# Optimization experiments

Hardware: AMD Instinct MI355X
Metric: run time of the kernel (lower is better)

## Reference

```python
import jax, jax.numpy as jnp
import numpy as np
from jax import lax

# config constants (match init_kwargs)
SEQ_LEN = 512
PRED_LEN = 96
ENC_IN = 64
D_MODEL = 128
E_LAYERS = 2
GRAPH_SCALE = 16
GRAPH_RANK = 8
TCN_KERNEL = 3
TCN_DILATION = 2
BATCH = 16


def setup_inputs() -> dict:
    key = jax.random.key(0)
    ks = jax.random.split(key, 12)
    s = 0.02
    inp = {
        "x_enc": jax.random.normal(ks[0], (BATCH, SEQ_LEN, ENC_IN), jnp.float32),
        "x_mark_enc": jnp.zeros((BATCH, SEQ_LEN, 4), jnp.float32),
        "x_dec": jnp.zeros((BATCH, PRED_LEN, ENC_IN), jnp.float32),
        "x_mark_dec": jnp.zeros((BATCH, PRED_LEN, 4), jnp.float32),
        # value embedding (scalar -> d_model)
        "w_emb": jax.random.normal(ks[1], (1, D_MODEL), jnp.float32) * s,
        "b_emb": jnp.zeros((D_MODEL,), jnp.float32),
        # stacked dilated causal conv layers [L, K, Cin, Cout]
        "conv_w": jax.random.normal(ks[2], (E_LAYERS, TCN_KERNEL, D_MODEL, D_MODEL), jnp.float32) * s,
        "conv_b": jnp.zeros((E_LAYERS, D_MODEL), jnp.float32),
        # low-rank graph generator projections
        "gg_w1": jax.random.normal(ks[3], (D_MODEL, GRAPH_RANK), jnp.float32) * s,
        "gg_b1": jnp.zeros((GRAPH_RANK,), jnp.float32),
        "gg_w2": jax.random.normal(ks[4], (D_MODEL, GRAPH_RANK), jnp.float32) * s,
        "gg_b2": jnp.zeros((GRAPH_RANK,), jnp.float32),
        # head: Linear(d_model * num_tokens, pred_len)
        "head_w": jax.random.normal(ks[5], (D_MODEL * SEQ_LEN, PRED_LEN), jnp.float32) * s,
        "head_b": jnp.zeros((PRED_LEN,), jnp.float32),
    }
    return inp


def _tcn(x_enc, w_emb, b_emb, conv_w, conv_b):
    # x_enc: [B, L, N] -> channel-independent per-variable encoding -> [B, N, L, D]
    B, L, N = x_enc.shape
    h = x_enc.transpose(0, 2, 1).reshape(B * N, L, 1) @ w_emb + b_emb  # [B*N, L, D]
    for i in range(conv_w.shape[0]):
        dil = TCN_DILATION ** i
        pad = (TCN_KERNEL - 1) * dil
        hp = jnp.pad(h, ((0, 0), (pad, 0), (0, 0)))  # causal left pad
        y = lax.conv_general_dilated(
            hp, conv_w[i], window_strides=(1,), padding="VALID",
            rhs_dilation=(dil,), dimension_numbers=("NWC", "WIO", "NWC"),
        ) + conv_b[i]
        h = jax.nn.gelu(y) + h  # residual
    return h.reshape(B, N, L, -1)


def _forward(x_enc, w_emb, b_emb, conv_w, conv_b, gg_w1, gg_b1, gg_w2, gg_b2, head_w, head_b):
    h_time = _tcn(x_enc, w_emb, b_emb, conv_w, conv_b)  # [B, N, L, D]
    B, N, L, D = h_time.shape
    S = L // GRAPH_SCALE  # number of segments (L divisible by scale)
    h_seg = h_time.reshape(B, N, S, GRAPH_SCALE, D)
    z = h_seg.mean(axis=3)  # [B, N, S, D] segment summaries
    # low-rank graph generation for all segments at once
    e1 = z @ gg_w1 + gg_b1  # [B, N, S, r]
    e2 = z @ gg_w2 + gg_b2
    scores = jnp.einsum("bnsr,bmsr->bsnm", e1, e2) / jnp.asarray(np.sqrt(GRAPH_RANK), z.dtype)
    adj = jax.nn.softmax(scores, axis=-1)  # [B, S, N, N] row-stochastic
    # adjacency temporal-smoothness regularizer: sum_s mean|adj_s - adj_{s-1}|
    reg = jnp.sum(jnp.mean(jnp.abs(adj[:, 1:] - adj[:, :-1]), axis=(0, 2, 3)))
    # graph-weighted feature mixing per segment
    h_mix = jnp.einsum("bsnm,bmscd->bnscd", adj, h_seg).reshape(B, N, L, D)
    # head over flattened (token, dim)
    out = h_mix.reshape(B, N, L * D) @ head_w + head_b  # [B, N, pred_len]
    return out.transpose(0, 2, 1), reg  # [B, pred_len, N]


def reference(x_enc, x_mark_enc, x_dec, x_mark_dec, w_emb, b_emb, conv_w, conv_b,
              gg_w1, gg_b1, gg_w2, gg_b2, head_w, head_b):
    # x_mark_enc / x_dec / x_mark_dec are unused by forecast path (faithful to source)
    return _forward(x_enc, w_emb, b_emb, conv_w, conv_b, gg_w1, gg_b1, gg_w2, gg_b2, head_w, head_b)
```

## Files before the change

### kernel.cpp

```cpp
#include <hip/hip_runtime.h>
#include <hip/hip_bf16.h>


#define BATCH 16
#define SEQ 512
#define NVAR 64
#define DM 128
#define SEG 32
#define SCL 16
#define RNK 8
#define PRED 96
#define BN (BATCH * NVAR)
#define ROWLEN (SEQ * DM)

typedef unsigned short ushort_t;
typedef __attribute__((ext_vector_type(8))) short short8;
typedef __attribute__((ext_vector_type(4))) float f32x4;

__device__ inline float bf2f(ushort_t u) {
    union { unsigned int i; float f; } x;
    x.i = ((unsigned int)u) << 16;
    return x.f;
}
__device__ inline ushort_t f2bf(float f) {
    union { float f; unsigned int i; } u;
    u.f = f;
    unsigned int x = u.i;
    return (ushort_t)((x + 0x7fffu + ((x >> 16) & 1u)) >> 16);
}
__device__ inline unsigned int pkbf(float a, float b) {
    __hip_bfloat162 h = __float22bfloat162_rn(make_float2(a, b));
    union { __hip_bfloat162 h2; unsigned int u; } c;
    c.h2 = h;
    return c.u;
}
__device__ inline float blo(unsigned int u) {
    union { unsigned int i; float f; } x;
    x.i = u << 16;
    return x.f;
}
__device__ inline float bhi(unsigned int u) {
    union { unsigned int i; float f; } x;
    x.i = u & 0xFFFF0000u;
    return x.f;
}
__device__ inline float gelu_fast(float x) {
    float x2 = x * x;
    float t2 = x * fmaf(-0.10294854f, x2, -2.3022584f);
    float e;
    asm("v_exp_f32 %0, %1" : "=v"(e) : "v"(t2));
    return x * __builtin_amdgcn_rcpf(1.0f + e);
}

__global__ __launch_bounds__(256) void prep(
    const float* __restrict__ conv_w, const float* __restrict__ w_emb,
    const float* __restrict__ b_emb, const float* __restrict__ conv_b,
    const float* __restrict__ head_w, const float* __restrict__ head_b,
    ushort_t* __restrict__ WTf, float* __restrict__ Acoef,
    float* __restrict__ Bias3, ushort_t* __restrict__ HWf,
    float* __restrict__ out, float* __restrict__ regacc) {
    __shared__ float ts[32 * 97];
    int bid = blockIdx.x;
    if (bid == 0 && threadIdx.x == 0) regacc[0] = 0.f;
    if (bid < 512) {
        int bx = bid >> 7, ci = bid & 127;
        if (threadIdx.x < 128) {
            int co = threadIdx.x;
            if (bx < 3) {
                int kt = ci >> 5, quad = (ci >> 3) & 3, j = ci & 7;
                int ng = co >> 4, col = co & 15;
                int lane = quad * 16 + col;
                WTf[((((size_t)bx * 4 + kt) * 8 + ng) * 64 + lane) * 8 + j] =
                    f2bf(conv_w[(size_t)(3 + bx) * 16384 + (size_t)ci * 128 + co]);
            } else if (ci == 0) {
                float a0 = 0.f, a1 = 0.f, a2 = 0.f, c0 = 0.f, c1 = 0.f, c2 = 0.f;
                for (int k = 0; k < 128; ++k) {
                    float we = w_emb[k], be = b_emb[k];
                    float w0 = conv_w[((size_t)(0 * 128 + k)) * 128 + co];
                    float w1 = conv_w[((size_t)(1 * 128 + k)) * 128 + co];
                    float w2 = conv_w[((size_t)(2 * 128 + k)) * 128 + co];
                    a0 += we * w0; c0 += be * w0;
                    a1 += we * w1; c1 += be * w1;
                    a2 += we * w2; c2 += be * w2;
                }
                Acoef[0 * 128 + co] = a0;
                Acoef[1 * 128 + co] = a1;
                Acoef[2 * 128 + co] = a2;
                float b0 = conv_b[co];
                Bias3[0 * 128 + co] = b0 + c2;
                Bias3[1 * 128 + co] = b0 + c1 + c2;
                Bias3[2 * 128 + co] = b0 + c0 + c1 + c2;
            }
        }
    } else if (bid < 2560) {
        int k32p = bid - 512;
        const float* src = head_w + (size_t)k32p * 32 * 96;
        for (int idx = threadIdx.x; idx < 3072; idx += 256) {
            int kk = idx / 96, p = idx - kk * 96;
            ts[kk * 97 + p] = src[idx];
        }
        __syncthreads();
        unsigned int* ob32 =
            reinterpret_cast<unsigned int*>(HWf + (size_t)k32p * 3072);
        for (int odx = threadIdx.x; odx < 1536; odx += 256) {
            int p = odx >> 4, kk = (odx & 15) * 2;
            ob32[odx] = pkbf(ts[kk * 97 + p], ts[(kk + 1) * 97 + p]);
        }
    } else {
        int idx = (bid - 2560) * 256 + threadIdx.x;
        if (idx < BATCH * PRED * NVAR) {
            int p = (idx >> 6) % PRED;
            out[idx] = head_b[p];
        }
    }
}

__global__ __launch_bounds__(256, 4) void tcn_mfma(
    const float* __restrict__ x, const float* __restrict__ w_emb,
    const float* __restrict__ b_emb, const float* __restrict__ Acoef,
    const float* __restrict__ Bias3, const ushort_t* __restrict__ WTf,
    const float* __restrict__ conv_b,
    const float* __restrict__ gw1, const float* __restrict__ gb1,
    const float* __restrict__ gw2, const float* __restrict__ gb2,
    ushort_t* __restrict__ h2, float* __restrict__ e1, float* __restrict__ e2) {
    __shared__ __align__(16) ushort_t h1s[68 * 136];
    __shared__ float xs[70];
    __shared__ float zbuf[4 * 136];

    int bn = blockIdx.x;
    int b = bn >> 6, n = bn & 63;
    int chunk = blockIdx.y;
    int l0 = chunk * 64;
    int tid = threadIdx.x;

    {
        const float* xb = x + (size_t)b * SEQ * NVAR + n;
        if (tid < 70) {
            int l = l0 - 6 + tid;
            xs[tid] = (l >= 0) ? xb[(size_t)l * NVAR] : 0.0f;
        }
    }
    __syncthreads();

    {
        int dp = (tid & 63) * 2;
        float2 A0 = *reinterpret_cast<const float2*>(&Acoef[0 * 128 + dp]);
        float2 A1 = *reinterpret_cast<const float2*>(&Acoef[1 * 128 + dp]);
        float2 A2 = *reinterpret_cast<const float2*>(&Acoef[2 * 128 + dp]);
        float2 BF = *reinterpret_cast<const float2*>(&Bias3[2 * 128 + dp]);
        float2 we2 = *reinterpret_cast<const float2*>(&w_emb[dp]);
        float2 be2 = *reinterpret_cast<const float2*>(&b_emb[dp]);
#pragma unroll
        for (int i = 0; i < 17; ++i) {
            int row = (tid >> 6) + 4 * i;
            int l = l0 - 4 + row;
            unsigned int pk = 0;
            if (l >= 0) {
                float x0 = xs[row], x1 = xs[row + 1], x2 = xs[row + 2];
                float2 bias = BF;
                if (l < 2)
                    bias = *reinterpret_cast<const float2*>(&Bias3[l * 128 + dp]);
                float y0 = fmaf(x0, A0.x, fmaf(x1, A1.x, fmaf(x2, A2.x, bias.x)));
                float y1 = fmaf(x0, A0.y, fmaf(x1, A1.y, fmaf(x2, A2.y, bias.y)));
                float r0 = gelu_fast(y0) + fmaf(x2, we2.x, be2.x);
                float r1 = gelu_fast(y1) + fmaf(x2, we2.y, be2.y);
                pk = pkbf(r0, r1);
            }
            *reinterpret_cast<unsigned int*>(&h1s[row * 136 + dp]) = pk;
        }
    }
    __syncthreads();

    int lane = tid & 63;
    int wv = tid >> 6;
    int quad = lane >> 4;
    int col = lane & 15;
    int cobase = wv * 32;

    f32x4 acc2[4][2];
#pragma unroll
    for (int mt = 0; mt < 4; ++mt)
#pragma unroll
        for (int nt = 0; nt < 2; ++nt)
            acc2[mt][nt] = (f32x4){0.f, 0.f, 0.f, 0.f};

#pragma unroll
    for (int tap = 0; tap < 3; ++tap) {
        short8 wf0[4], wf1[4];
#pragma unroll
        for (int kt = 0; kt < 4; ++kt) {
            const ushort_t* bp =
                WTf + ((((size_t)tap * 4 + kt) * 8 + wv * 2) * 64 + lane) * 8;
            wf0[kt] = *(const short8*)bp;
            wf1[kt] = *(const short8*)(bp + 512);
        }
#pragma unroll
        for (int kt = 0; kt < 4; ++kt) {
            int kc = kt * 32 + quad * 8;
#pragma unroll
            for (int mt = 0; mt < 4; ++mt) {
                short8 hf = *(const short8*)&h1s[(mt * 16 + col + 2 * tap) * 136 + kc];
                acc2[mt][0] = __builtin_amdgcn_mfma_f32_16x16x32_bf16(wf0[kt], hf, acc2[mt][0], 0, 0, 0);
                acc2[mt][1] = __builtin_amdgcn_mfma_f32_16x16x32_bf16(wf1[kt], hf, acc2[mt][1], 0, 0, 0);
            }
        }
    }

    {
        uint2 res[4][2];
#pragma unroll
        for (int mt = 0; mt < 4; ++mt) {
            int li = mt * 16 + col;
#pragma unroll
            for (int nt = 0; nt < 2; ++nt) {
                int co = cobase + nt * 16 + quad * 4;
                res[mt][nt] = *reinterpret_cast<const uint2*>(
                    &h1s[(li + 4) * 136 + co]);
            }
        }
        __syncthreads();
        float4 bias[2];
        bias[0] = *reinterpret_cast<const float4*>(&conv_b[DM + cobase + quad * 4]);
        bias[1] = *reinterpret_cast<const float4*>(&conv_b[DM + cobase + 16 + quad * 4]);
#pragma unroll
        for (int mt = 0; mt < 4; ++mt) {
            int li = mt * 16 + col;
#pragma unroll
            for (int nt = 0; nt < 2; ++nt) {
                int co = cobase + nt * 16 + quad * 4;
                float h0 = gelu_fast(acc2[mt][nt][0] + bias[nt].x) + blo(res[mt][nt].x);
                float h1 = gelu_fast(acc2[mt][nt][1] + bias[nt].y) + bhi(res[mt][nt].x);
                float h2v = gelu_fast(acc2[mt][nt][2] + bias[nt].z) + blo(res[mt][nt].y);
                float h3 = gelu_fast(acc2[mt][nt][3] + bias[nt].w) + bhi(res[mt][nt].y);
                uint2 pk;
                pk.x = pkbf(h0, h1);
                pk.y = pkbf(h2v, h3);
                *reinterpret_cast<uint2*>(&h1s[li * 136 + co]) = pk;
            }
        }
    }
    __syncthreads();

    {
        ushort_t* orow = h2 + (size_t)bn * ROWLEN + (size_t)l0 * 128;
#pragma unroll
        for (int i = 0; i < 4; ++i) {
            int q = tid + 256 * i;
            int row = q >> 4, c8 = (q & 15) * 8;
            *(short8*)&orow[row * 128 + c8] = *(const short8*)&h1s[row * 136 + c8];
        }
    }
    {
        int sl = tid >> 6;
        int dp = (tid & 63) * 2;
        float a0 = 0.0f, a1 = 0.0f;
#pragma unroll
        for (int c = 0; c < SCL; ++c) {
            unsigned int u = *reinterpret_cast<const unsigned int*>(
                &h1s[(sl * 16 + c) * 136 + dp]);
            a0 += blo(u);
            a1 += bhi(u);
        }
        zbuf[sl * 136 + dp] = a0 * 0.0625f;
        zbuf[sl * 136 + dp + 1] = a1 * 0.0625f;
    }
    __syncthreads();
    {
        int outi = tid >> 2;
        int part = tid & 3;
        int sl = outi >> 4;
        int which = (outi >> 3) & 1;
        int r = outi & 7;
        const float* w = which ? gw2 : gw1;
        float a = 0.0f;
#pragma unroll 8
        for (int i = 0; i < 32; ++i) {
            int d = i * 4 + part;
            a += zbuf[sl * 136 + d] * w[d * RNK + r];
        }
        a += __shfl_xor(a, 1, 64);
        a += __shfl_xor(a, 2, 64);
        if (part == 0) {
            a += (which ? gb2 : gb1)[r];
            int s = chunk * 4 + sl;
            (which ? e2 : e1)[(((size_t)b * SEG + s) * NVAR + n) * RNK + r] = a;
        }
    }
}

__global__ __launch_bounds__(256) void g_out(
    const ushort_t* __restrict__ h2, const ushort_t* __restrict__ HWf,
    const float* __restrict__ e1, const float* __restrict__ e2,
    float* __restrict__ out, float* __restrict__ regacc) {
    __shared__ __align__(16) ushort_t As[2][64 * 72];
    __shared__ __align__(16) float Gs[96][66];
    __shared__ float e1s[2][64][9];
    __shared__ float e2s[2][64][9];
    __shared__ float wsum[4];
    float* adjn = reinterpret_cast<float*>(As);

    int b = blockIdx.x, s = blockIdx.y;
    int tid = threadIdx.x;
    int lane = tid & 63, wv = tid >> 6;
    int quad = lane >> 4, col = lane & 15;
    int mh = wv & 1;
    int ph = wv >> 1;
    int p0 = ph * 48 + col;

    for (int idx = tid; idx < 1024; idx += 256) {
        int j = idx >> 9, mm = (idx >> 3) & 63, r = idx & 7;
        int ss = s - 1 + j;
        float v1 = 0.f, v2 = 0.f;
        if (ss >= 0) {
            size_t o = (((size_t)b * SEG + ss) * NVAR + mm) * RNK + r;
            v1 = e1[o];
            v2 = e2[o];
        }
        e1s[j][mm][r] = v1;
        e2s[j][mm][r] = v2;
    }

    int arow = tid >> 2, akq = (tid & 3) * 16;
    const ushort_t* aptr =
        h2 + (size_t)(b * 64 + arow) * ROWLEN + (size_t)s * 2048 + akq;
    const ushort_t* hb =
        HWf + (size_t)s * 196608 + (size_t)p0 * 32 + quad * 8;

    f32x4 acc[3][2];
#pragma unroll
    for (int i = 0; i < 3; ++i)
#pragma unroll
        for (int j = 0; j < 2; ++j) acc[i][j] = (f32x4){0.f, 0.f, 0.f, 0.f};

    short8 pa0 = *(const short8*)aptr;
    short8 pa1 = *(const short8*)(aptr + 8);
    short8 pf[2][2][3];
#pragma unroll
    for (int kk = 0; kk < 2; ++kk)
#pragma unroll
        for (int i = 0; i < 3; ++i)
            pf[0][kk][i] = *(const short8*)(hb + kk * 3072 + i * 512);
    *(short8*)&As[0][arow * 72 + akq] = pa0;
    *(short8*)&As[0][arow * 72 + akq + 8] = pa1;
    __syncthreads();

#pragma unroll
    for (int kt = 0; kt < 32; ++kt) {
        const int par = kt & 1;
        if (kt < 31) {
            const ushort_t* ap = aptr + (kt + 1) * 64;
            pa0 = *(const short8*)ap;
            pa1 = *(const short8*)(ap + 8);
            const ushort_t* fb = hb + (size_t)(kt + 1) * 6144;
#pragma unroll
            for (int kk = 0; kk < 2; ++kk)
#pragma unroll
                for (int i = 0; i < 3; ++i)
                    pf[par ^ 1][kk][i] =
                        *(const short8*)(fb + kk * 3072 + i * 512);
        }
#pragma unroll
        for (int kk = 0; kk < 2; ++kk) {
            int kc = kk * 32 + quad * 8;
#pragma unroll
            for (int j = 0; j < 2; ++j) {
                short8 bnfr =
                    *(const short8*)&As[par][(mh * 32 + j * 16 + col) * 72 + kc];
#pragma unroll
                for (int i = 0; i < 3; ++i)
                    acc[i][j] = __builtin_amdgcn_mfma_f32_16x16x32_bf16(
                        pf[par][kk][i], bnfr, acc[i][j], 0, 0, 0);
            }
        }
        if (kt < 31) {
            *(short8*)&As[par ^ 1][arow * 72 + akq] = pa0;
            *(short8*)&As[par ^ 1][arow * 72 + akq + 8] = pa1;
        }
        __syncthreads();
    }

#pragma unroll
    for (int i = 0; i < 3; ++i)
#pragma unroll
        for (int j = 0; j < 2; ++j)
#pragma unroll
            for (int r = 0; r < 4; ++r)
                Gs[ph * 48 + i * 16 + quad * 4 + r][mh * 32 + j * 16 + col] =
                    acc[i][j][r];

    float regsum = 0.0f;
    for (int t = 0; t < 16; ++t) {
        int nl = wv * 16 + t;
        float scC = 0.0f, scP = 0.0f;
#pragma unroll
        for (int r = 0; r < 8; ++r) {
            scC += e1s[1][nl][r] * e2s[1][lane][r];
            scP += e1s[0][nl][r] * e2s[0][lane][r];
        }
        scC *= 0.35355339059327373f;
        scP *= 0.35355339059327373f;
        float mxC = scC, mxP = scP;
        for (int off = 32; off; off >>= 1) {
            mxC = fmaxf(mxC, __shfl_xor(mxC, off, 64));
            mxP = fmaxf(mxP, __shfl_xor(mxP, off, 64));
        }
        float exC = __expf(scC - mxC), exP = __expf(scP - mxP);
        float smC = exC, smP = exP;
        for (int off = 32; off; off >>= 1) {
            smC += __shfl_xor(smC, off, 64);
            smP += __shfl_xor(smP, off, 64);
        }
        float aC = exC * __builtin_amdgcn_rcpf(smC);
        if (s > 0) regsum += fabsf(aC - exP * __builtin_amdgcn_rcpf(smP));
        adjn[nl * 66 + lane] = aC;
    }
    __syncthreads();

    {
        int pg = tid >> 4;
        int ng = tid & 15;
        float ao[6][4];
#pragma unroll
        for (int j = 0; j < 6; ++j)
#pragma unroll
            for (int i = 0; i < 4; ++i) ao[j][i] = 0.f;
#pragma unroll 4
        for (int m = 0; m < 64; m += 2) {
            float2 av[4];
#pragma unroll
            for (int i = 0; i < 4; ++i)
                av[i] = *reinterpret_cast<const float2*>(
                    &adjn[(ng * 4 + i) * 66 + m]);
#pragma unroll
            for (int j = 0; j < 6; ++j) {
                float2 g = *reinterpret_cast<const float2*>(&Gs[pg * 6 + j][m]);
#pragma unroll
                for (int i = 0; i < 4; ++i)
                    ao[j][i] = fmaf(g.x, av[i].x, fmaf(g.y, av[i].y, ao[j][i]));
            }
        }
#pragma unroll
        for (int j = 0; j < 6; ++j)
#pragma unroll
            for (int i = 0; i < 4; ++i)
                atomicAdd(&out[((size_t)b * PRED + pg * 6 + j) * NVAR +
                               ng * 4 + i],
                          ao[j][i]);
    }
    for (int off = 32; off; off >>= 1) regsum += __shfl_xor(regsum, off, 64);
    if (lane == 0) wsum[wv] = regsum;
    __syncthreads();
    if (tid == 0)
        atomicAdd(regacc, wsum[0] + wsum[1] + wsum[2] + wsum[3]);
}

__global__ void fin(const float* __restrict__ regacc, float* __restrict__ out,
                    int out_size) {
    out[out_size - 1] = regacc[0] * (1.0f / 65536.0f);
}

extern "C" void kernel_launch(void* const* d_in, const int* in_sizes, int n_in,
                              void* d_out, int out_size, void* d_ws,
                              size_t ws_size, hipStream_t stream) {
    const float* x_enc  = (const float*)d_in[0];
    const float* w_emb  = (const float*)d_in[4];
    const float* b_emb  = (const float*)d_in[5];
    const float* conv_w = (const float*)d_in[6];
    const float* conv_b = (const float*)d_in[7];
    const float* gg_w1  = (const float*)d_in[8];
    const float* gg_b1  = (const float*)d_in[9];
    const float* gg_w2  = (const float*)d_in[10];
    const float* gg_b2  = (const float*)d_in[11];
    const float* head_w = (const float*)d_in[12];
    const float* head_b = (const float*)d_in[13];
    float* out = (float*)d_out;

    char* ws = (char*)d_ws;
    ushort_t* h2   = (ushort_t*)(ws);
    float* e1      = (float*)(ws + 134217728);
    float* e2      = (float*)(ws + 135266304);
    ushort_t* WTf  = (ushort_t*)(ws + 136314880);
    float* Acoef   = (float*)(ws + 136413184);
    float* Bias3   = (float*)(ws + 136414720);
    ushort_t* HWf  = (ushort_t*)(ws + 136416256);
    float* regacc  = (float*)(ws + 157286400);

    prep<<<2944, 256, 0, stream>>>(
        conv_w, w_emb, b_emb, conv_b, head_w, head_b,
        WTf, Acoef, Bias3, HWf, out, regacc);
    tcn_mfma<<<dim3(BN, SEQ / 64), 256, 0, stream>>>(
        x_enc, w_emb, b_emb, Acoef, Bias3, WTf, conv_b,
        gg_w1, gg_b1, gg_w2, gg_b2, h2, e1, e2);
    g_out<<<dim3(BATCH, SEG), 256, 0, stream>>>(
        h2, HWf, e1, e2, out, regacc);
    fin<<<1, 1, 0, stream>>>(regacc, out, out_size);
}
```

Baseline: 307.9 us.

## Move head-weight conversion into TCN launch and double K tile in g_out

The head_w transpose and bf16 conversion, along with the output bias init, move out of the prep kernel into extra grid rows (y=8,9) of the TCN kernel. This leaves prep as a small conv-weight kernel and lets the head-weight work overlap with TCN compute. In g_out the K step per iteration doubles from 64 to 128, halving barrier count at the cost of more registers and shared memory. The grid is also flattened to 1D with segment-fastest ordering. The extra blocks in the TCN grid share its LDS allocation and launch bounds.

```diff
diff --git a/kernel.cpp b/kernel.cpp
--- a/kernel.cpp
+++ b/kernel.cpp
@@ -52,66 +52,39 @@
     return x * __builtin_amdgcn_rcpf(1.0f + e);
 }
 
-__global__ __launch_bounds__(256) void prep(
+__global__ __launch_bounds__(128) void prep_wt(
     const float* __restrict__ conv_w, const float* __restrict__ w_emb,
     const float* __restrict__ b_emb, const float* __restrict__ conv_b,
-    const float* __restrict__ head_w, const float* __restrict__ head_b,
     ushort_t* __restrict__ WTf, float* __restrict__ Acoef,
-    float* __restrict__ Bias3, ushort_t* __restrict__ HWf,
-    float* __restrict__ out, float* __restrict__ regacc) {
-    __shared__ float ts[32 * 97];
+    float* __restrict__ Bias3, float* __restrict__ regacc) {
     int bid = blockIdx.x;
     if (bid == 0 && threadIdx.x == 0) regacc[0] = 0.f;
-    if (bid < 512) {
-        int bx = bid >> 7, ci = bid & 127;
-        if (threadIdx.x < 128) {
-            int co = threadIdx.x;
-            if (bx < 3) {
-                int kt = ci >> 5, quad = (ci >> 3) & 3, j = ci & 7;
-                int ng = co >> 4, col = co & 15;
-                int lane = quad * 16 + col;
-                WTf[((((size_t)bx * 4 + kt) * 8 + ng) * 64 + lane) * 8 + j] =
-                    f2bf(conv_w[(size_t)(3 + bx) * 16384 + (size_t)ci * 128 + co]);
-            } else if (ci == 0) {
-                float a0 = 0.f, a1 = 0.f, a2 = 0.f, c0 = 0.f, c1 = 0.f, c2 = 0.f;
-                for (int k = 0; k < 128; ++k) {
-                    float we = w_emb[k], be = b_emb[k];
-                    float w0 = conv_w[((size_t)(0 * 128 + k)) * 128 + co];
-                    float w1 = conv_w[((size_t)(1 * 128 + k)) * 128 + co];
-                    float w2 = conv_w[((size_t)(2 * 128 + k)) * 128 + co];
-                    a0 += we * w0; c0 += be * w0;
-                    a1 += we * w1; c1 += be * w1;
-                    a2 += we * w2; c2 += be * w2;
-                }
-                Acoef[0 * 128 + co] = a0;
-                Acoef[1 * 128 + co] = a1;
-                Acoef[2 * 128 + co] = a2;
-                float b0 = conv_b[co];
-                Bias3[0 * 128 + co] = b0 + c2;
-                Bias3[1 * 128 + co] = b0 + c1 + c2;
-                Bias3[2 * 128 + co] = b0 + c0 + c1 + c2;
-            }
-        }
-    } else if (bid < 2560) {
-        int k32p = bid - 512;
-        const float* src = head_w + (size_t)k32p * 32 * 96;
-        for (int idx = threadIdx.x; idx < 3072; idx += 256) {
-            int kk = idx / 96, p = idx - kk * 96;
-            ts[kk * 97 + p] = src[idx];
-        }
-        __syncthreads();
-        unsigned int* ob32 =
-            reinterpret_cast<unsigned int*>(HWf + (size_t)k32p * 3072);
-        for (int odx = threadIdx.x; odx < 1536; odx += 256) {
-            int p = odx >> 4, kk = (odx & 15) * 2;
-            ob32[odx] = pkbf(ts[kk * 97 + p], ts[(kk + 1) * 97 + p]);
-        }
-    } else {
-        int idx = (bid - 2560) * 256 + threadIdx.x;
-        if (idx < BATCH * PRED * NVAR) {
-            int p = (idx >> 6) % PRED;
-            out[idx] = head_b[p];
-        }
+    int bx = bid >> 7, ci = bid & 127;
+    int co = threadIdx.x;
+    if (bx < 3) {
+        int kt = ci >> 5, quad = (ci >> 3) & 3, j = ci & 7;
+        int ng = co >> 4, col = co & 15;
+        int lane = quad * 16 + col;
+        WTf[((((size_t)bx * 4 + kt) * 8 + ng) * 64 + lane) * 8 + j] =
+            f2bf(conv_w[(size_t)(3 + bx) * 16384 + (size_t)ci * 128 + co]);
+    } else if (ci == 0) {
+        float a0 = 0.f, a1 = 0.f, a2 = 0.f, c0 = 0.f, c1 = 0.f, c2 = 0.f;
+        for (int k = 0; k < 128; ++k) {
+            float we = w_emb[k], be = b_emb[k];
+            float w0 = conv_w[((size_t)(0 * 128 + k)) * 128 + co];
+            float w1 = conv_w[((size_t)(1 * 128 + k)) * 128 + co];
+            float w2 = conv_w[((size_t)(2 * 128 + k)) * 128 + co];
+            a0 += we * w0; c0 += be * w0;
+            a1 += we * w1; c1 += be * w1;
+            a2 += we * w2; c2 += be * w2;
+        }
+        Acoef[0 * 128 + co] = a0;
+        Acoef[1 * 128 + co] = a1;
+        Acoef[2 * 128 + co] = a2;
+        float b0 = conv_b[co];
+        Bias3[0 * 128 + co] = b0 + c2;
+        Bias3[1 * 128 + co] = b0 + c1 + c2;
+        Bias3[2 * 128 + co] = b0 + c0 + c1 + c2;
     }
 }
 
@@ -122,16 +95,49 @@
     const float* __restrict__ conv_b,
     const float* __restrict__ gw1, const float* __restrict__ gb1,
     const float* __restrict__ gw2, const float* __restrict__ gb2,
-    ushort_t* __restrict__ h2, float* __restrict__ e1, float* __restrict__ e2) {
+    const float* __restrict__ head_w, const float* __restrict__ head_b,
+    ushort_t* __restrict__ h2, float* __restrict__ e1, float* __restrict__ e2,
+    ushort_t* __restrict__ HWf, float* __restrict__ out) {
     __shared__ __align__(16) ushort_t h1s[68 * 136];
     __shared__ float xs[70];
     __shared__ float zbuf[4 * 136];
+
+    int tid = threadIdx.x;
+
+    if (blockIdx.y == 8) {
+        float* ts = reinterpret_cast<float*>(h1s);
+#pragma unroll
+        for (int u = 0; u < 2; ++u) {
+            int k32p = blockIdx.x * 2 + u;
+            const float* src = head_w + (size_t)k32p * 3072;
+            for (int idx = tid; idx < 3072; idx += 256) {
+                int kk = idx / 96, p = idx - kk * 96;
+                ts[kk * 97 + p] = src[idx];
+            }
+            __syncthreads();
+            unsigned int* ob32 =
+                reinterpret_cast<unsigned int*>(HWf + (size_t)k32p * 3072);
+            for (int odx = tid; odx < 1536; odx += 256) {
+                int p = odx >> 4, kk = (odx & 15) * 2;
+                ob32[odx] = pkbf(ts[kk * 97 + p], ts[(kk + 1) * 97 + p]);
+            }
+            __syncthreads();
+        }
+        return;
+    }
+    if (blockIdx.y == 9) {
+        int idx = blockIdx.x * 256 + tid;
+        if (blockIdx.x < 384 && idx < BATCH * PRED * NVAR) {
+            int p = (idx >> 6) % PRED;
+            out[idx] = head_b[p];
+        }
+        return;
+    }
 
     int bn = blockIdx.x;
     int b = bn >> 6, n = bn & 63;
     int chunk = blockIdx.y;
     int l0 = chunk * 64;
-    int tid = threadIdx.x;
 
     {
         const float* xb = x + (size_t)b * SEQ * NVAR + n;
@@ -292,14 +298,15 @@
     const ushort_t* __restrict__ h2, const ushort_t* __restrict__ HWf,
     const float* __restrict__ e1, const float* __restrict__ e2,
     float* __restrict__ out, float* __restrict__ regacc) {
-    __shared__ __align__(16) ushort_t As[2][64 * 72];
+    __shared__ __align__(16) ushort_t As[2][64 * 136];
     __shared__ __align__(16) float Gs[96][66];
     __shared__ float e1s[2][64][9];
     __shared__ float e2s[2][64][9];
     __shared__ float wsum[4];
     float* adjn = reinterpret_cast<float*>(As);
 
-    int b = blockIdx.x, s = blockIdx.y;
+    int bid = blockIdx.x;
+    int s = bid & 31, b = bid >> 5;
     int tid = threadIdx.x;
     int lane = tid & 63, wv = tid >> 6;
     int quad = lane >> 4, col = lane & 15;
@@ -320,7 +327,8 @@
         e2s[j][mm][r] = v2;
     }
 
-    int arow = tid >> 2, akq = (tid & 3) * 16;
+    int arow = tid >> 2;
+    int akq = (tid & 3) * 32;
     const ushort_t* aptr =
         h2 + (size_t)(b * 64 + arow) * ROWLEN + (size_t)s * 2048 + akq;
     const ushort_t* hb =
@@ -332,49 +340,59 @@
 #pragma unroll
         for (int j = 0; j < 2; ++j) acc[i][j] = (f32x4){0.f, 0.f, 0.f, 0.f};
 
-    short8 pa0 = *(const short8*)aptr;
-    short8 pa1 = *(const short8*)(aptr + 8);
-    short8 pf[2][2][3];
-#pragma unroll
-    for (int kk = 0; kk < 2; ++kk)
-#pragma unroll
-        for (int i = 0; i < 3; ++i)
-            pf[0][kk][i] = *(const short8*)(hb + kk * 3072 + i * 512);
-    *(short8*)&As[0][arow * 72 + akq] = pa0;
-    *(short8*)&As[0][arow * 72 + akq + 8] = pa1;
-    __syncthreads();
-
-#pragma unroll
-    for (int kt = 0; kt < 32; ++kt) {
-        const int par = kt & 1;
-        if (kt < 31) {
-            const ushort_t* ap = aptr + (kt + 1) * 64;
-            pa0 = *(const short8*)ap;
-            pa1 = *(const short8*)(ap + 8);
-            const ushort_t* fb = hb + (size_t)(kt + 1) * 6144;
-#pragma unroll
-            for (int kk = 0; kk < 2; ++kk)
-#pragma unroll
-                for (int i = 0; i < 3; ++i)
-                    pf[par ^ 1][kk][i] =
-                        *(const short8*)(fb + kk * 3072 + i * 512);
-        }
-#pragma unroll
-        for (int kk = 0; kk < 2; ++kk) {
-            int kc = kk * 32 + quad * 8;
-#pragma unroll
-            for (int j = 0; j < 2; ++j) {
-                short8 bnfr =
-                    *(const short8*)&As[par][(mh * 32 + j * 16 + col) * 72 + kc];
-#pragma unroll
-                for (int i = 0; i < 3; ++i)
-                    acc[i][j] = __builtin_amdgcn_mfma_f32_16x16x32_bf16(
-                        pf[par][kk][i], bnfr, acc[i][j], 0, 0, 0);
-            }
-        }
-        if (kt < 31) {
-            *(short8*)&As[par ^ 1][arow * 72 + akq] = pa0;
-            *(short8*)&As[par ^ 1][arow * 72 + akq + 8] = pa1;
+    short8 pa[4];
+    short8 pf[2][2][2][3];
+#pragma unroll
+    for (int j = 0; j < 4; ++j) pa[j] = *(const short8*)(aptr + j * 8);
+#pragma unroll
+    for (int tk = 0; tk < 2; ++tk)
+#pragma unroll
+        for (int kk = 0; kk < 2; ++kk)
+#pragma unroll
+            for (int i = 0; i < 3; ++i)
+                pf[0][tk][kk][i] =
+                    *(const short8*)(hb + tk * 6144 + kk * 3072 + i * 512);
+#pragma unroll
+    for (int j = 0; j < 4; ++j)
+        *(short8*)&As[0][arow * 136 + akq + j * 8] = pa[j];
+    __syncthreads();
+
+#pragma unroll
+    for (int t = 0; t < 16; ++t) {
+        const int par = t & 1;
+        if (t < 15) {
+            const ushort_t* ap = aptr + (t + 1) * 128;
+#pragma unroll
+            for (int j = 0; j < 4; ++j) pa[j] = *(const short8*)(ap + j * 8);
+            const ushort_t* fb = hb + (size_t)(t + 1) * 12288;
+#pragma unroll
+            for (int tk = 0; tk < 2; ++tk)
+#pragma unroll
+                for (int kk = 0; kk < 2; ++kk)
+#pragma unroll
+                    for (int i = 0; i < 3; ++i)
+                        pf[par ^ 1][tk][kk][i] = *(const short8*)(
+                            fb + tk * 6144 + kk * 3072 + i * 512);
+        }
+#pragma unroll
+        for (int tk = 0; tk < 2; ++tk)
+#pragma unroll
+            for (int kk = 0; kk < 2; ++kk) {
+                int kc = tk * 64 + kk * 32 + quad * 8;
+#pragma unroll
+                for (int j = 0; j < 2; ++j) {
+                    short8 bnfr = *(const short8*)&As[par][
+                        (mh * 32 + j * 16 + col) * 136 + kc];
+#pragma unroll
+                    for (int i = 0; i < 3; ++i)
+                        acc[i][j] = __builtin_amdgcn_mfma_f32_16x16x32_bf16(
+                            pf[par][tk][kk][i], bnfr, acc[i][j], 0, 0, 0);
+                }
+            }
+        if (t < 15) {
+#pragma unroll
+            for (int j = 0; j < 4; ++j)
+                *(short8*)&As[par ^ 1][arow * 136 + akq + j * 8] = pa[j];
         }
         __syncthreads();
     }
@@ -485,13 +503,11 @@
     ushort_t* HWf  = (ushort_t*)(ws + 136416256);
     float* regacc  = (float*)(ws + 157286400);
 
-    prep<<<2944, 256, 0, stream>>>(
-        conv_w, w_emb, b_emb, conv_b, head_w, head_b,
-        WTf, Acoef, Bias3, HWf, out, regacc);
-    tcn_mfma<<<dim3(BN, SEQ / 64), 256, 0, stream>>>(
+    prep_wt<<<512, 128, 0, stream>>>(
+        conv_w, w_emb, b_emb, conv_b, WTf, Acoef, Bias3, regacc);
+    tcn_mfma<<<dim3(BN, 10), 256, 0, stream>>>(
         x_enc, w_emb, b_emb, Acoef, Bias3, WTf, conv_b,
-        gg_w1, gg_b1, gg_w2, gg_b2, h2, e1, e2);
-    g_out<<<dim3(BATCH, SEG), 256, 0, stream>>>(
-        h2, HWf, e1, e2, out, regacc);
+        gg_w1, gg_b1, gg_w2, gg_b2, head_w, head_b, h2, e1, e2, HWf, out);
+    g_out<<<512, 256, 0, stream>>>(h2, HWf, e1, e2, out, regacc);
     fin<<<1, 1, 0, stream>>>(regacc, out, out_size);
 }
```

New measurement: 303.9 us. Within noise of the previous version (-1.3%).

## Load g_out A operand directly from global into registers, drop LDS staging

Applied to the files above, without the earlier changes.

The g_out GEMM no longer stages the h2 tile through double-buffered shared memory. Each wave loads its MFMA B-fragments straight from global memory into registers, with a two-deep register prefetch over 16 larger k-steps. This removes the per-iteration LDS writes and barriers, and the launch grid is flattened to 1D with the segment index varying fastest. In exchange, each h2 element is now read by more than one wave, which raises global/L2 traffic and register pressure.

```diff
diff --git a/kernel.cpp b/kernel.cpp
--- a/kernel.cpp
+++ b/kernel.cpp
@@ -292,14 +292,14 @@
     const ushort_t* __restrict__ h2, const ushort_t* __restrict__ HWf,
     const float* __restrict__ e1, const float* __restrict__ e2,
     float* __restrict__ out, float* __restrict__ regacc) {
-    __shared__ __align__(16) ushort_t As[2][64 * 72];
     __shared__ __align__(16) float Gs[96][66];
+    __shared__ __align__(16) float adjn[64][66];
     __shared__ float e1s[2][64][9];
     __shared__ float e2s[2][64][9];
     __shared__ float wsum[4];
-    float* adjn = reinterpret_cast<float*>(As);
-
-    int b = blockIdx.x, s = blockIdx.y;
+
+    int bid = blockIdx.x;
+    int s = bid & 31, b = bid >> 5;
     int tid = threadIdx.x;
     int lane = tid & 63, wv = tid >> 6;
     int quad = lane >> 4, col = lane & 15;
@@ -320,9 +320,9 @@
         e2s[j][mm][r] = v2;
     }
 
-    int arow = tid >> 2, akq = (tid & 3) * 16;
-    const ushort_t* aptr =
-        h2 + (size_t)(b * 64 + arow) * ROWLEN + (size_t)s * 2048 + akq;
+    const ushort_t* a0 = h2 +
+        (size_t)(b * 64 + mh * 32 + col) * ROWLEN + (size_t)s * 2048 + quad * 8;
+    const ushort_t* a1 = a0 + (size_t)16 * ROWLEN;
     const ushort_t* hb =
         HWf + (size_t)s * 196608 + (size_t)p0 * 32 + quad * 8;
 
@@ -332,51 +332,53 @@
 #pragma unroll
         for (int j = 0; j < 2; ++j) acc[i][j] = (f32x4){0.f, 0.f, 0.f, 0.f};
 
-    short8 pa0 = *(const short8*)aptr;
-    short8 pa1 = *(const short8*)(aptr + 8);
-    short8 pf[2][2][3];
-#pragma unroll
-    for (int kk = 0; kk < 2; ++kk)
-#pragma unroll
-        for (int i = 0; i < 3; ++i)
-            pf[0][kk][i] = *(const short8*)(hb + kk * 3072 + i * 512);
-    *(short8*)&As[0][arow * 72 + akq] = pa0;
-    *(short8*)&As[0][arow * 72 + akq + 8] = pa1;
-    __syncthreads();
-
-#pragma unroll
-    for (int kt = 0; kt < 32; ++kt) {
-        const int par = kt & 1;
-        if (kt < 31) {
-            const ushort_t* ap = aptr + (kt + 1) * 64;
-            pa0 = *(const short8*)ap;
-            pa1 = *(const short8*)(ap + 8);
-            const ushort_t* fb = hb + (size_t)(kt + 1) * 6144;
-#pragma unroll
-            for (int kk = 0; kk < 2; ++kk)
-#pragma unroll
-                for (int i = 0; i < 3; ++i)
-                    pf[par ^ 1][kk][i] =
-                        *(const short8*)(fb + kk * 3072 + i * 512);
-        }
+    short8 pa[2][2][4];
+    short8 pf[2][2][2][3];
+#pragma unroll
+    for (int tk = 0; tk < 2; ++tk)
 #pragma unroll
         for (int kk = 0; kk < 2; ++kk) {
-            int kc = kk * 32 + quad * 8;
-#pragma unroll
-            for (int j = 0; j < 2; ++j) {
-                short8 bnfr =
-                    *(const short8*)&As[par][(mh * 32 + j * 16 + col) * 72 + kc];
-#pragma unroll
-                for (int i = 0; i < 3; ++i)
-                    acc[i][j] = __builtin_amdgcn_mfma_f32_16x16x32_bf16(
-                        pf[par][kk][i], bnfr, acc[i][j], 0, 0, 0);
-            }
-        }
-        if (kt < 31) {
-            *(short8*)&As[par ^ 1][arow * 72 + akq] = pa0;
-            *(short8*)&As[par ^ 1][arow * 72 + akq + 8] = pa1;
-        }
-        __syncthreads();
+            int ko = tk * 64 + kk * 32;
+            pa[0][0][tk * 2 + kk] = *(const short8*)(a0 + ko);
+            pa[0][1][tk * 2 + kk] = *(const short8*)(a1 + ko);
+#pragma unroll
+            for (int i = 0; i < 3; ++i)
+                pf[0][tk][kk][i] =
+                    *(const short8*)(hb + tk * 6144 + kk * 3072 + i * 512);
+        }
+
+#pragma unroll
+    for (int t = 0; t < 16; ++t) {
+        const int par = t & 1;
+        if (t < 15) {
+            const ushort_t* an0 = a0 + (t + 1) * 128;
+            const ushort_t* an1 = a1 + (t + 1) * 128;
+            const ushort_t* fb = hb + (size_t)(t + 1) * 12288;
+#pragma unroll
+            for (int tk = 0; tk < 2; ++tk)
+#pragma unroll
+                for (int kk = 0; kk < 2; ++kk) {
+                    int ko = tk * 64 + kk * 32;
+                    pa[par ^ 1][0][tk * 2 + kk] = *(const short8*)(an0 + ko);
+                    pa[par ^ 1][1][tk * 2 + kk] = *(const short8*)(an1 + ko);
+#pragma unroll
+                    for (int i = 0; i < 3; ++i)
+                        pf[par ^ 1][tk][kk][i] = *(const short8*)(
+                            fb + tk * 6144 + kk * 3072 + i * 512);
+                }
+        }
+#pragma unroll
+        for (int tk = 0; tk < 2; ++tk)
+#pragma unroll
+            for (int kk = 0; kk < 2; ++kk) {
+                const int f = tk * 2 + kk;
+#pragma unroll
+                for (int j = 0; j < 2; ++j)
+#pragma unroll
+                    for (int i = 0; i < 3; ++i)
+                        acc[i][j] = __builtin_amdgcn_mfma_f32_16x16x32_bf16(
+                            pf[par][tk][kk][i], pa[par][j][f], acc[i][j], 0, 0, 0);
+            }
     }
 
 #pragma unroll
@@ -387,6 +389,7 @@
             for (int r = 0; r < 4; ++r)
                 Gs[ph * 48 + i * 16 + quad * 4 + r][mh * 32 + j * 16 + col] =
                     acc[i][j][r];
+    __syncthreads();
 
     float regsum = 0.0f;
     for (int t = 0; t < 16; ++t) {
@@ -412,7 +415,7 @@
         }
         float aC = exC * __builtin_amdgcn_rcpf(smC);
         if (s > 0) regsum += fabsf(aC - exP * __builtin_amdgcn_rcpf(smP));
-        adjn[nl * 66 + lane] = aC;
+        adjn[nl][lane] = aC;
     }
     __syncthreads();
 
@@ -430,7 +433,7 @@
 #pragma unroll
             for (int i = 0; i < 4; ++i)
                 av[i] = *reinterpret_cast<const float2*>(
-                    &adjn[(ng * 4 + i) * 66 + m]);
+                    &adjn[ng * 4 + i][m]);
 #pragma unroll
             for (int j = 0; j < 6; ++j) {
                 float2 g = *reinterpret_cast<const float2*>(&Gs[pg * 6 + j][m]);
@@ -491,7 +494,6 @@
     tcn_mfma<<<dim3(BN, SEQ / 64), 256, 0, stream>>>(
         x_enc, w_emb, b_emb, Acoef, Bias3, WTf, conv_b,
         gg_w1, gg_b1, gg_w2, gg_b2, h2, e1, e2);
-    g_out<<<dim3(BATCH, SEG), 256, 0, stream>>>(
-        h2, HWf, e1, e2, out, regacc);
+    g_out<<<512, 256, 0, stream>>>(h2, HWf, e1, e2, out, regacc);
     fin<<<1, 1, 0, stream>>>(regacc, out, out_size);
 }
```

New measurement: 327.6 us. 6.4% more time.

## Split g_out reduction over two K halves to double grid size

Applied to the files above, without the earlier changes.

The g_out kernel now launches 1024 blocks instead of 512, with each block handling half of a segment's K range (kh). It uses 128-wide K tiles with a 136-element stride, and the Gs, As and adjn buffers share one shared-memory region. The e2 values are held in registers rather than shared memory, and the previous-segment softmax used for the regularizer is computed only by the kh==0 block. The goal is more parallelism and better CU occupancy on the head GEMM. In exchange, the adjacency softmax is computed twice and out receives twice as many atomic adds.

```diff
diff --git a/kernel.cpp b/kernel.cpp
--- a/kernel.cpp
+++ b/kernel.cpp
@@ -292,14 +292,16 @@
     const ushort_t* __restrict__ h2, const ushort_t* __restrict__ HWf,
     const float* __restrict__ e1, const float* __restrict__ e2,
     float* __restrict__ out, float* __restrict__ regacc) {
-    __shared__ __align__(16) ushort_t As[2][64 * 72];
-    __shared__ __align__(16) float Gs[96][66];
+    __shared__ __align__(16) char smem[42240];
     __shared__ float e1s[2][64][9];
-    __shared__ float e2s[2][64][9];
     __shared__ float wsum[4];
-    float* adjn = reinterpret_cast<float*>(As);
-
-    int b = blockIdx.x, s = blockIdx.y;
+    ushort_t* As0 = reinterpret_cast<ushort_t*>(smem);
+    ushort_t* As1 = As0 + 64 * 136;
+    float* Gs = reinterpret_cast<float*>(smem);
+    float* adjn = reinterpret_cast<float*>(smem + 25344);
+
+    int bid = blockIdx.x;
+    int s = bid & 31, b = (bid >> 5) & 15, kh = bid >> 9;
     int tid = threadIdx.x;
     int lane = tid & 63, wv = tid >> 6;
     int quad = lane >> 4, col = lane & 15;
@@ -307,24 +309,35 @@
     int ph = wv >> 1;
     int p0 = ph * 48 + col;
 
+    float e2r[2][8];
+#pragma unroll
+    for (int j = 0; j < 2; ++j) {
+        int ss = s - 1 + j;
+        if (ss >= 0) {
+            const float* p =
+                &e2[(((size_t)b * SEG + ss) * NVAR + lane) * RNK];
+            float4 v0 = *reinterpret_cast<const float4*>(p);
+            float4 v1 = *reinterpret_cast<const float4*>(p + 4);
+            e2r[j][0] = v0.x; e2r[j][1] = v0.y; e2r[j][2] = v0.z; e2r[j][3] = v0.w;
+            e2r[j][4] = v1.x; e2r[j][5] = v1.y; e2r[j][6] = v1.z; e2r[j][7] = v1.w;
+        } else {
+#pragma unroll
+            for (int r = 0; r < 8; ++r) e2r[j][r] = 0.0f;
+        }
+    }
     for (int idx = tid; idx < 1024; idx += 256) {
-        int j = idx >> 9, mm = (idx >> 3) & 63, r = idx & 7;
+        int j = idx >> 9, nl = (idx >> 3) & 63, r = idx & 7;
         int ss = s - 1 + j;
-        float v1 = 0.f, v2 = 0.f;
-        if (ss >= 0) {
-            size_t o = (((size_t)b * SEG + ss) * NVAR + mm) * RNK + r;
-            v1 = e1[o];
-            v2 = e2[o];
-        }
-        e1s[j][mm][r] = v1;
-        e2s[j][mm][r] = v2;
-    }
-
-    int arow = tid >> 2, akq = (tid & 3) * 16;
-    const ushort_t* aptr =
-        h2 + (size_t)(b * 64 + arow) * ROWLEN + (size_t)s * 2048 + akq;
-    const ushort_t* hb =
-        HWf + (size_t)s * 196608 + (size_t)p0 * 32 + quad * 8;
+        e1s[j][nl][r] = (ss >= 0)
+            ? e1[(((size_t)b * SEG + ss) * NVAR + nl) * RNK + r] : 0.0f;
+    }
+
+    int arow = tid >> 2;
+    int akq = (tid & 3) * 32;
+    const ushort_t* aptr = h2 +
+        (size_t)(b * 64 + arow) * ROWLEN + (size_t)s * 2048 + kh * 1024 + akq;
+    const ushort_t* hb = HWf +
+        (size_t)s * 196608 + (size_t)kh * 98304 + (size_t)p0 * 32 + quad * 8;
 
     f32x4 acc[3][2];
 #pragma unroll
@@ -332,49 +345,61 @@
 #pragma unroll
         for (int j = 0; j < 2; ++j) acc[i][j] = (f32x4){0.f, 0.f, 0.f, 0.f};
 
-    short8 pa0 = *(const short8*)aptr;
-    short8 pa1 = *(const short8*)(aptr + 8);
+    short8 pa[4];
     short8 pf[2][2][3];
+#pragma unroll
+    for (int j = 0; j < 4; ++j) pa[j] = *(const short8*)(aptr + j * 8);
 #pragma unroll
     for (int kk = 0; kk < 2; ++kk)
 #pragma unroll
         for (int i = 0; i < 3; ++i)
             pf[0][kk][i] = *(const short8*)(hb + kk * 3072 + i * 512);
-    *(short8*)&As[0][arow * 72 + akq] = pa0;
-    *(short8*)&As[0][arow * 72 + akq + 8] = pa1;
-    __syncthreads();
-
-#pragma unroll
-    for (int kt = 0; kt < 32; ++kt) {
-        const int par = kt & 1;
-        if (kt < 31) {
-            const ushort_t* ap = aptr + (kt + 1) * 64;
-            pa0 = *(const short8*)ap;
-            pa1 = *(const short8*)(ap + 8);
-            const ushort_t* fb = hb + (size_t)(kt + 1) * 6144;
-#pragma unroll
-            for (int kk = 0; kk < 2; ++kk)
-#pragma unroll
-                for (int i = 0; i < 3; ++i)
-                    pf[par ^ 1][kk][i] =
-                        *(const short8*)(fb + kk * 3072 + i * 512);
-        }
-#pragma unroll
-        for (int kk = 0; kk < 2; ++kk) {
-            int kc = kk * 32 + quad * 8;
-#pragma unroll
-            for (int j = 0; j < 2; ++j) {
-                short8 bnfr =
-                    *(const short8*)&As[par][(mh * 32 + j * 16 + col) * 72 + kc];
-#pragma unroll
-                for (int i = 0; i < 3; ++i)
-                    acc[i][j] = __builtin_amdgcn_mfma_f32_16x16x32_bf16(
-                        pf[par][kk][i], bnfr, acc[i][j], 0, 0, 0);
-            }
-        }
-        if (kt < 31) {
-            *(short8*)&As[par ^ 1][arow * 72 + akq] = pa0;
-            *(short8*)&As[par ^ 1][arow * 72 + akq + 8] = pa1;
+#pragma unroll
+    for (int j = 0; j < 4; ++j)
+        *(short8*)&As0[arow * 136 + akq + j * 8] = pa[j];
+    __syncthreads();
+
+#pragma unroll
+    for (int t = 0; t < 8; ++t) {
+        const int par = t & 1;
+        if (t < 7) {
+            const ushort_t* ap = aptr + (t + 1) * 128;
+#pragma unroll
+            for (int j = 0; j < 4; ++j) pa[j] = *(const short8*)(ap + j * 8);
+        }
+#pragma unroll
+        for (int tk = 0; tk < 2; ++tk) {
+            const int hp = t * 2 + tk;
+            const int pp = hp & 1;
+            if (hp < 15) {
+                const ushort_t* fb = hb + (size_t)(hp + 1) * 6144;
+#pragma unroll
+                for (int kk = 0; kk < 2; ++kk)
+#pragma unroll
+                    for (int i = 0; i < 3; ++i)
+                        pf[pp ^ 1][kk][i] =
+                            *(const short8*)(fb + kk * 3072 + i * 512);
+            }
+            const ushort_t* asb = par ? As1 : As0;
+#pragma unroll
+            for (int kk = 0; kk < 2; ++kk) {
+                int kc = tk * 64 + kk * 32 + quad * 8;
+#pragma unroll
+                for (int j = 0; j < 2; ++j) {
+                    short8 bnfr = *(const short8*)&asb[
+                        (mh * 32 + j * 16 + col) * 136 + kc];
+#pragma unroll
+                    for (int i = 0; i < 3; ++i)
+                        acc[i][j] = __builtin_amdgcn_mfma_f32_16x16x32_bf16(
+                            pf[pp][kk][i], bnfr, acc[i][j], 0, 0, 0);
+                }
+            }
+        }
+        if (t < 7) {
+            ushort_t* asn = par ? As0 : As1;
+#pragma unroll
+            for (int j = 0; j < 4; ++j)
+                *(short8*)&asn[arow * 136 + akq + j * 8] = pa[j];
         }
         __syncthreads();
     }
@@ -385,34 +410,37 @@
         for (int j = 0; j < 2; ++j)
 #pragma unroll
             for (int r = 0; r < 4; ++r)
-                Gs[ph * 48 + i * 16 + quad * 4 + r][mh * 32 + j * 16 + col] =
-                    acc[i][j][r];
+                Gs[(ph * 48 + i * 16 + quad * 4 + r) * 66 +
+                   mh * 32 + j * 16 + col] = acc[i][j][r];
 
     float regsum = 0.0f;
     for (int t = 0; t < 16; ++t) {
         int nl = wv * 16 + t;
-        float scC = 0.0f, scP = 0.0f;
-#pragma unroll
-        for (int r = 0; r < 8; ++r) {
-            scC += e1s[1][nl][r] * e2s[1][lane][r];
-            scP += e1s[0][nl][r] * e2s[0][lane][r];
-        }
+        float scC = 0.0f;
+#pragma unroll
+        for (int r = 0; r < 8; ++r) scC += e1s[1][nl][r] * e2r[1][r];
         scC *= 0.35355339059327373f;
-        scP *= 0.35355339059327373f;
-        float mxC = scC, mxP = scP;
-        for (int off = 32; off; off >>= 1) {
+        float mxC = scC;
+        for (int off = 32; off; off >>= 1)
             mxC = fmaxf(mxC, __shfl_xor(mxC, off, 64));
-            mxP = fmaxf(mxP, __shfl_xor(mxP, off, 64));
-        }
-        float exC = __expf(scC - mxC), exP = __expf(scP - mxP);
-        float smC = exC, smP = exP;
-        for (int off = 32; off; off >>= 1) {
-            smC += __shfl_xor(smC, off, 64);
-            smP += __shfl_xor(smP, off, 64);
-        }
+        float exC = __expf(scC - mxC);
+        float smC = exC;
+        for (int off = 32; off; off >>= 1) smC += __shfl_xor(smC, off, 64);
         float aC = exC * __builtin_amdgcn_rcpf(smC);
-        if (s > 0) regsum += fabsf(aC - exP * __builtin_amdgcn_rcpf(smP));
         adjn[nl * 66 + lane] = aC;
+        if (kh == 0 && s > 0) {
+            float scP = 0.0f;
+#pragma unroll
+            for (int r = 0; r < 8; ++r) scP += e1s[0][nl][r] * e2r[0][r];
+            scP *= 0.35355339059327373f;
+            float mxP = scP;
+            for (int off = 32; off; off >>= 1)
+                mxP = fmaxf(mxP, __shfl_xor(mxP, off, 64));
+            float exP = __expf(scP - mxP);
+            float smP = exP;
+            for (int off = 32; off; off >>= 1) smP += __shfl_xor(smP, off, 64);
+            regsum += fabsf(aC - exP * __builtin_amdgcn_rcpf(smP));
+        }
     }
     __syncthreads();
 
@@ -433,7 +461,8 @@
                     &adjn[(ng * 4 + i) * 66 + m]);
 #pragma unroll
             for (int j = 0; j < 6; ++j) {
-                float2 g = *reinterpret_cast<const float2*>(&Gs[pg * 6 + j][m]);
+                float2 g = *reinterpret_cast<const float2*>(
+                    &Gs[(pg * 6 + j) * 66 + m]);
 #pragma unroll
                 for (int i = 0; i < 4; ++i)
                     ao[j][i] = fmaf(g.x, av[i].x, fmaf(g.y, av[i].y, ao[j][i]));
@@ -450,7 +479,7 @@
     for (int off = 32; off; off >>= 1) regsum += __shfl_xor(regsum, off, 64);
     if (lane == 0) wsum[wv] = regsum;
     __syncthreads();
-    if (tid == 0)
+    if (tid == 0 && kh == 0)
         atomicAdd(regacc, wsum[0] + wsum[1] + wsum[2] + wsum[3]);
 }
 
@@ -491,7 +520,6 @@
     tcn_mfma<<<dim3(BN, SEQ / 64), 256, 0, stream>>>(
         x_enc, w_emb, b_emb, Acoef, Bias3, WTf, conv_b,
         gg_w1, gg_b1, gg_w2, gg_b2, h2, e1, e2);
-    g_out<<<dim3(BATCH, SEG), 256, 0, stream>>>(
-        h2, HWf, e1, e2, out, regacc);
+    g_out<<<1024, 256, 0, stream>>>(h2, HWf, e1, e2, out, regacc);
     fin<<<1, 1, 0, stream>>>(regacc, out, out_size);
 }
```

Measured after the change: 355.8 us. +15.6%, slower.
